# Kernel tuning notes

Hardware: AMD Instinct MI355X
Metric: run time of the kernel (lower is better)

The kernel has to match this reference:

```python
import jax, jax.numpy as jnp
import numpy as np

B, L, D = 256, 512, 768


def setup_inputs() -> dict:
    key = jax.random.key(0)
    k1, k2, k3, k4, k5, k6 = jax.random.split(key, 6)
    final_hidden = jax.random.normal(k1, (B, L, D), dtype=jnp.float32)
    attention_mask = jax.random.randint(k2, (B, L), 0, 2, dtype=jnp.int32)
    W13 = jax.random.normal(k3, (13, 4, D), dtype=jnp.float32) * 0.02
    b13 = jax.random.normal(k4, (13, 4), dtype=jnp.float32) * 0.02
    W14 = jax.random.normal(k5, (2, D), dtype=jnp.float32) * 0.02
    b14 = jax.random.normal(k6, (2,), dtype=jnp.float32) * 0.02
    return {"final_hidden": final_hidden, "attention_mask": attention_mask,
            "W13": W13, "b13": b13, "W14": W14, "b14": b14}


def reference(final_hidden, attention_mask, W13, b13, W14, b14):
    # Fused masked mean pooling: zero out padded positions, sum over seq,
    # divide by per-row valid-token count (replaces the per-element loops).
    mask = attention_mask.astype(final_hidden.dtype)            # [B, L]
    pooled = jnp.einsum('bl,bld->bd', mask, final_hidden)       # [B, D]
    pooled = pooled / mask.sum(axis=1, keepdims=True)           # [B, D]
    # 13 heads of out-dim 4 (batched as one einsum) + one head of out-dim 2.
    out13 = jnp.einsum('bd,kod->bko', pooled, W13) + b13        # [B, 13, 4]
    out14 = pooled @ W14.T + b14                                # [B, 2]
    # Original returns a list of 14 tensors; we concat along the last dim
    # ([B, 13*4 + 2] = [B, 54]) which preserves all values.
    return jnp.concatenate([out13.reshape(out13.shape[0], -1), out14], axis=-1)
```

## Files before the change

kernel.cpp:

```cpp
#include <hip/hip_runtime.h>

#define BATCH 256
#define SEQ   512
#define DIM   768
#define D4    (DIM / 4)
#define NOUT  54

__global__ __launch_bounds__(1024) void bow_fused_kernel(
    const float* __restrict__ fh, const int* __restrict__ mask,
    const float* __restrict__ W13, const float* __restrict__ b13,
    const float* __restrict__ W14, const float* __restrict__ b14,
    float* __restrict__ out)
{
    const int b    = blockIdx.x;
    const int tid  = threadIdx.x;
    const int lane = tid & 63;
    const int wave = tid >> 6;

    __shared__ unsigned long long balls[8];
    __shared__ int   list[SEQ];
    __shared__ float pooled[DIM];

    int my_m = 0;
    if (wave < 8) {
        my_m = mask[b * SEQ + tid];
        unsigned long long bl = __ballot(my_m != 0);
        if (lane == 0) balls[wave] = bl;
    }
    __syncthreads();

    int n = 0;
    #pragma unroll
    for (int w = 0; w < 8; ++w) n += __popcll(balls[w]);

    if (wave < 8 && my_m != 0) {
        int off = 0;
        for (int w = 0; w < wave; ++w) off += __popcll(balls[w]);
        const unsigned long long bl = balls[wave];
        list[off + __popcll(bl & ((1ull << lane) - 1))] = tid;
    }
    __syncthreads();

    const float4* fh4 = (const float4*)fh + (size_t)b * SEQ * D4;

    float4 a0 = make_float4(0.f, 0.f, 0.f, 0.f);
    float4 a1 = a0, a2 = a0;

    int i = wave;
    for (; i + 16 < n; i += 32) {
        const float4* r0 = fh4 + (size_t)list[i]      * D4;
        const float4* r1 = fh4 + (size_t)list[i + 16] * D4;
        float4 x0 = r0[lane], x1 = r0[lane + 64], x2 = r0[lane + 128];
        float4 y0 = r1[lane], y1 = r1[lane + 64], y2 = r1[lane + 128];
        a0.x += x0.x + y0.x; a0.y += x0.y + y0.y;
        a0.z += x0.z + y0.z; a0.w += x0.w + y0.w;
        a1.x += x1.x + y1.x; a1.y += x1.y + y1.y;
        a1.z += x1.z + y1.z; a1.w += x1.w + y1.w;
        a2.x += x2.x + y2.x; a2.y += x2.y + y2.y;
        a2.z += x2.z + y2.z; a2.w += x2.w + y2.w;
    }
    if (i < n) {
        const float4* r0 = fh4 + (size_t)list[i] * D4;
        float4 x0 = r0[lane], x1 = r0[lane + 64], x2 = r0[lane + 128];
        a0.x += x0.x; a0.y += x0.y; a0.z += x0.z; a0.w += x0.w;
        a1.x += x1.x; a1.y += x1.y; a1.z += x1.z; a1.w += x1.w;
        a2.x += x2.x; a2.y += x2.y; a2.z += x2.z; a2.w += x2.w;
    }

    __shared__ float4 red[16][D4];
    red[wave][lane]       = a0;
    red[wave][lane + 64]  = a1;
    red[wave][lane + 128] = a2;
    __syncthreads();

    const float inv = 1.0f / (float)n;
    if (tid < D4) {
        float4 acc = make_float4(0.f, 0.f, 0.f, 0.f);
        #pragma unroll
        for (int w = 0; w < 16; ++w) {
            float4 v = red[w][tid];
            acc.x += v.x; acc.y += v.y; acc.z += v.z; acc.w += v.w;
        }
        ((float4*)pooled)[tid] =
            make_float4(acc.x * inv, acc.y * inv, acc.z * inv, acc.w * inv);
    }
    __syncthreads();

    for (int o = wave; o < NOUT; o += 16) {
        const float* Wrow = (o < 52) ? (W13 + (size_t)o * DIM)
                                     : (W14 + (size_t)(o - 52) * DIM);
        const float bias  = (o < 52) ? b13[o] : b14[o - 52];
        float acc = 0.f;
        #pragma unroll
        for (int j = 0; j < 12; ++j) {
            const int d = lane + 64 * j;
            acc = fmaf(pooled[d], Wrow[d], acc);
        }
        for (int off = 32; off; off >>= 1) acc += __shfl_down(acc, off);
        if (lane == 0) out[(size_t)b * NOUT + o] = acc + bias;
    }
}

extern "C" void kernel_launch(void* const* d_in, const int* in_sizes, int n_in,
                              void* d_out, int out_size, void* d_ws, size_t ws_size,
                              hipStream_t stream) {
    const float* fh   = (const float*)d_in[0];
    const int*   mask = (const int*)d_in[1];
    const float* W13  = (const float*)d_in[2];
    const float* b13  = (const float*)d_in[3];
    const float* W14  = (const float*)d_in[4];
    const float* b14  = (const float*)d_in[5];
    float*       out  = (float*)d_out;

    bow_fused_kernel<<<dim3(BATCH), dim3(1024), 0, stream>>>(
        fh, mask, W13, b13, W14, b14, out);
}
```

Before: 487.9 us.

## Split pooling into strip-partial kernel plus head kernel for more parallelism

```diff
diff --git a/kernel.cpp b/kernel.cpp
--- a/kernel.cpp
+++ b/kernel.cpp
@@ -5,6 +5,116 @@
 #define DIM   768
 #define D4    (DIM / 4)
 #define NOUT  54
+
+#define STRIPS        8
+#define ROWS_PER_STRIP (SEQ / STRIPS)
+#define NPART         (BATCH * STRIPS)
+
+__global__ __launch_bounds__(256) void pool_partial_kernel(
+    const float* __restrict__ fh, const int* __restrict__ mask,
+    float* __restrict__ part, int* __restrict__ cnt)
+{
+    const int bid  = blockIdx.x;
+    const int b    = bid >> 3;
+    const int s    = bid & 7;
+    const int tid  = threadIdx.x;
+    const int lane = tid & 63;
+    const int wave = tid >> 6;
+
+    const int row0 = s * ROWS_PER_STRIP + wave * 16;
+
+    int m = 0;
+    if (lane < 16) m = mask[b * SEQ + row0 + lane];
+
+    const float4* fh4 = (const float4*)fh + ((size_t)b * SEQ + row0) * D4;
+
+    float4 a0 = make_float4(0.f, 0.f, 0.f, 0.f);
+    float4 a1 = a0, a2 = a0;
+
+    #pragma unroll
+    for (int r = 0; r < 16; ++r) {
+        if (__shfl(m, r) != 0) {
+            const float4* rp = fh4 + (size_t)r * D4;
+            float4 x0 = rp[lane], x1 = rp[lane + 64], x2 = rp[lane + 128];
+            a0.x += x0.x; a0.y += x0.y; a0.z += x0.z; a0.w += x0.w;
+            a1.x += x1.x; a1.y += x1.y; a1.z += x1.z; a1.w += x1.w;
+            a2.x += x2.x; a2.y += x2.y; a2.z += x2.z; a2.w += x2.w;
+        }
+    }
+
+    const int myc = __popcll(__ballot(m != 0));
+
+    __shared__ float4 red[4][D4];
+    __shared__ int    wc[4];
+    red[wave][lane]       = a0;
+    red[wave][lane + 64]  = a1;
+    red[wave][lane + 128] = a2;
+    if (lane == 0) wc[wave] = myc;
+    __syncthreads();
+
+    if (tid < D4) {
+        float4 v0 = red[0][tid], v1 = red[1][tid];
+        float4 v2 = red[2][tid], v3 = red[3][tid];
+        float4 acc;
+        acc.x = (v0.x + v1.x) + (v2.x + v3.x);
+        acc.y = (v0.y + v1.y) + (v2.y + v3.y);
+        acc.z = (v0.z + v1.z) + (v2.z + v3.z);
+        acc.w = (v0.w + v1.w) + (v2.w + v3.w);
+        ((float4*)part)[(size_t)bid * D4 + tid] = acc;
+    }
+    if (tid == 0) cnt[bid] = wc[0] + wc[1] + wc[2] + wc[3];
+}
+
+__global__ __launch_bounds__(256) void head_kernel(
+    const float* __restrict__ part, const int* __restrict__ cnt,
+    const float* __restrict__ W13, const float* __restrict__ b13,
+    const float* __restrict__ W14, const float* __restrict__ b14,
+    float* __restrict__ out)
+{
+    const int b    = blockIdx.x;
+    const int tid  = threadIdx.x;
+    const int lane = tid & 63;
+    const int wave = tid >> 6;
+
+    __shared__ float pooled[DIM];
+    __shared__ int   ns;
+
+    if (tid < 8) {
+        int n = cnt[b * 8 + tid];
+        n += __shfl_down(n, 4);
+        n += __shfl_down(n, 2);
+        n += __shfl_down(n, 1);
+        if (tid == 0) ns = n;
+    }
+
+    if (tid < D4) {
+        const float4* p4 = (const float4*)part + (size_t)b * 8 * D4;
+        float4 acc = make_float4(0.f, 0.f, 0.f, 0.f);
+        #pragma unroll
+        for (int s = 0; s < 8; ++s) {
+            float4 v = p4[(size_t)s * D4 + tid];
+            acc.x += v.x; acc.y += v.y; acc.z += v.z; acc.w += v.w;
+        }
+        ((float4*)pooled)[tid] = acc;
+    }
+    __syncthreads();
+
+    const float inv = 1.0f / (float)ns;
+
+    for (int o = wave; o < NOUT; o += 4) {
+        const float* Wrow = (o < 52) ? (W13 + (size_t)o * DIM)
+                                     : (W14 + (size_t)(o - 52) * DIM);
+        const float bias  = (o < 52) ? b13[o] : b14[o - 52];
+        float acc = 0.f;
+        #pragma unroll
+        for (int j = 0; j < 12; ++j) {
+            const int d = lane + 64 * j;
+            acc = fmaf(pooled[d], Wrow[d], acc);
+        }
+        for (int off = 32; off; off >>= 1) acc += __shfl_down(acc, off);
+        if (lane == 0) out[(size_t)b * NOUT + o] = fmaf(acc, inv, bias);
+    }
+}
 
 __global__ __launch_bounds__(1024) void bow_fused_kernel(
     const float* __restrict__ fh, const int* __restrict__ mask,
@@ -112,6 +222,19 @@
     const float* b14  = (const float*)d_in[5];
     float*       out  = (float*)d_out;
 
-    bow_fused_kernel<<<dim3(BATCH), dim3(1024), 0, stream>>>(
-        fh, mask, W13, b13, W14, b14, out);
-}
+    const size_t part_bytes = (size_t)NPART * DIM * sizeof(float);
+    const size_t cnt_bytes  = (size_t)NPART * sizeof(int);
+
+    if (d_ws != nullptr && ws_size >= part_bytes + cnt_bytes) {
+        float* part = (float*)d_ws;
+        int*   cnt  = (int*)((char*)d_ws + part_bytes);
+
+        pool_partial_kernel<<<dim3(NPART), dim3(256), 0, stream>>>(
+            fh, mask, part, cnt);
+        head_kernel<<<dim3(BATCH), dim3(256), 0, stream>>>(
+            part, cnt, W13, b13, W14, b14, out);
+    } else {
+        bow_fused_kernel<<<dim3(BATCH), dim3(1024), 0, stream>>>(
+            fh, mask, W13, b13, W14, b14, out);
+    }
+}
```

Result: slower. 502.0 us (+2.9%).
